# Kernel optimization log

Hardware: AMD Instinct MI355X
Metric: run time of the kernel (lower is better)

## Reference

```python
import jax, jax.numpy as jnp
import numpy as np

TEMPERATURE = 0.05


def setup_inputs() -> dict:
    key = jax.random.key(0)
    k1, k2, k3 = jax.random.split(key, 3)
    B, L, D = 4096, 32, 768
    image_features = jax.random.normal(k1, (B, D), dtype=jnp.float32)
    text_features = jax.random.normal(k2, (B, D), dtype=jnp.float32)
    labels = jax.random.randint(k3, (B, L), 0, 2, dtype=jnp.int64)
    return {"image_features": image_features, "text_features": text_features, "labels": labels}


def reference(image_features, text_features, labels):
    B, L = labels.shape
    num_logits = B
    # mask[i, j] = 1.0 iff labels[i, j] != 0; y[j] = outer(mask[:, j], mask[:, j])
    mask = (labels != 0).astype(jnp.float32)  # [B, L]
    # logit_scale = F.normalize(ones(L), p=2) * log(1/temp) -> every entry equal
    s = jnp.log(jnp.float32(1.0 / TEMPERATURE)) / jnp.sqrt(jnp.float32(L))
    logits_per_image = image_features @ text_features.T  # [B, B]
    logits_per_text = logits_per_image.T
    # All L scaled slices are identical (scale vector is constant), so one log_softmax each.
    pred_1 = jax.nn.log_softmax(s * logits_per_image, axis=-1)  # [B, B]
    pred_2 = jax.nn.log_softmax(s * logits_per_text, axis=-1)
    # kl_div(pred, y_j, 'sum') with 0/1 targets = -sum(y_j * pred)
    # sum_j m[:,j]^T P m[:,j] computed via two GEMMs without materializing [L,B,B]
    def masked_sum(pred):
        return jnp.einsum('jb,bj->', mask.T @ pred, mask)  # scalar
    loss_a = -masked_sum(pred_1) / num_logits
    loss_b = -masked_sum(pred_2) / num_logits
    total_loss = (loss_a + loss_b) / 2.0
    return total_loss / L
```

## Files before the change

kernel.cpp:

```cpp
#include <hip/hip_runtime.h>

#define NB 4096
#define DK 768
#define DKB 768
#define SCALE_S 0.5295756522f

typedef float f32x4 __attribute__((ext_vector_type(4)));
typedef int i32x4 __attribute__((ext_vector_type(4)));
typedef int i32x8 __attribute__((ext_vector_type(8)));

#define OFF_XQ      0u
#define OFF_YQ      3145728u
#define OFF_ROWPM   12582912u
#define OFF_ROWPS   13107200u
#define OFF_COLPM   13631488u
#define OFF_COLPS   14155776u
#define OFF_BITS    14712832u
#define OFF_CSPART  14729216u
#define OFF_DOTP    14731264u
#define OFF_WSUM    14735360u

static __device__ __forceinline__ unsigned char f2e4m3(float f) {
  union { float f; unsigned u; } x; x.f = f;
  unsigned s = (x.u >> 24) & 0x80u;
  x.u &= 0x7FFFFFFFu;
  float af = x.f;
  if (af >= 448.f) return (unsigned char)(s | 0x7Eu);
  int e = (int)(x.u >> 23) - 127;
  int eq = e < -6 ? -6 : e;
  float scale = __int_as_float((unsigned)((3 - eq) + 127) << 23);
  int q = (int)rintf(af * scale);
  if (q == 16) { q = 8; ++eq; }
  if (e < -6) return (unsigned char)(s | (unsigned)q);
  return (unsigned char)(s | (((unsigned)(eq + 7)) << 3) | ((unsigned)(q - 8)));
}

static __device__ __forceinline__ void gload16(const void* g, void* l) {
  __builtin_amdgcn_global_load_lds(
      (const __attribute__((address_space(1))) unsigned int*)g,
      (__attribute__((address_space(3))) unsigned int*)l,
      16, 0, 0);
}

__global__ void k_prep(const int* __restrict__ labels, unsigned* __restrict__ bits,
                       int* __restrict__ csPart,
                       const float* __restrict__ X, const float* __restrict__ Y,
                       unsigned char* __restrict__ Xq, unsigned char* __restrict__ Yq) {
  int t = threadIdx.x;
  if (blockIdx.x < 16) {
    __shared__ int cs[32];
    if (t < 32) cs[t] = 0;
    __syncthreads();
    int i = blockIdx.x * 256 + t;
    const int* row = labels + (size_t)i * 32;
    unsigned b = 0;
#pragma unroll
    for (int j = 0; j < 32; ++j) if (row[j] != 0) b |= (1u << j);
    bits[i] = b;
#pragma unroll
    for (int j = 0; j < 32; ++j) if (b & (1u << j)) atomicAdd(&cs[j], 1);
    __syncthreads();
    if (t < 32) csPart[blockIdx.x * 32 + t] = cs[t];
  } else {
    const int N4 = (NB * DK) / 4;
    const int stride = (gridDim.x - 16) * 256;
    for (int idx = (blockIdx.x - 16) * 256 + t; idx < 2 * N4; idx += stride) {
      float4 v; unsigned* dst;
      if (idx < N4) { v = ((const float4*)X)[idx]; dst = (unsigned*)Xq + idx; }
      else          { v = ((const float4*)Y)[idx - N4]; dst = (unsigned*)Yq + (idx - N4); }
      unsigned p = (unsigned)f2e4m3(v.x) | ((unsigned)f2e4m3(v.y) << 8) |
                   ((unsigned)f2e4m3(v.z) << 16) | ((unsigned)f2e4m3(v.w) << 24);
      *dst = p;
    }
  }
}


#define STAGE_T(DBUF, KT) do { \
    char* _lb = lds + (DBUF) * 65536 + lbOff; \
    const unsigned char* _g = pG + (size_t)(KT) * 128; \
    gload16(_g,                      _lb); \
    gload16(_g + (size_t)64  * DKB,  _lb + 8192); \
    gload16(_g + (size_t)128 * DKB,  _lb + 16384); \
    gload16(_g + (size_t)192 * DKB,  _lb + 24576); \
  } while (0)

#define LOADFRAG(DST, BASE) do { \
    i32x4 _lo = *(const i32x4*)((BASE) + offg0); \
    i32x4 _hi = *(const i32x4*)((BASE) + offg1); \
    DST[0] = _lo[0]; DST[1] = _lo[1]; DST[2] = _lo[2]; DST[3] = _lo[3]; \
    DST[4] = _hi[0]; DST[5] = _hi[1]; DST[6] = _hi[2]; DST[7] = _hi[3]; \
  } while (0)

__launch_bounds__(1024)
__global__ void k_gemm(const unsigned char* __restrict__ Xq,
                       const unsigned char* __restrict__ Yq,
                       const unsigned* __restrict__ bits,
                       float* __restrict__ rowPM, float* __restrict__ rowPS,
                       float* __restrict__ colPM, float* __restrict__ colPS,
                       float* __restrict__ dotPart) {
  extern __shared__ char lds[];

  const int t = threadIdx.x;
  const int wave = t >> 6, lane = t & 63;
  const int wr = wave >> 2, wc = wave & 3;

  const int bid = blockIdx.x;
  const int xcd = bid & 7, loc = bid >> 3;
  const int rb = (xcd & 3) * 4 + (loc >> 3);
  const int cb = (xcd >> 2) * 8 + (loc & 7);

  const int g0 = ((lane & 7) ^ (lane >> 3)) * 16;
  const int srow = (wave & 7) * 8 + (lane >> 3);
  const unsigned char* pG = (wave < 8)
      ? Xq + (size_t)(rb * 256 + srow) * DKB + g0
      : Yq + (size_t)(cb * 256 + srow) * DKB + g0;
  const int lbOff = ((wave < 8) ? 0 : 32768) + (wave & 7) * 1024;

  const int lrow = lane & 15;
  const int s7 = lrow & 7;
  const int gp = (lane >> 4) * 2;
  const int offg0 = ((gp) ^ s7) * 16;
  const int offg1 = ((gp + 1) ^ s7) * 16;
  const int rowA0 = (wr * 64 + lrow) * 128;
  const int rowB0 = 32768 + (wc * 64 + lrow) * 128;

  f32x4 acc[4][4];
#pragma unroll
  for (int m = 0; m < 4; ++m)
#pragma unroll
    for (int n = 0; n < 4; ++n) acc[m][n] = (f32x4){0.f, 0.f, 0.f, 0.f};

  STAGE_T(0, 0);
  asm volatile("s_waitcnt vmcnt(0)" ::: "memory");
  __builtin_amdgcn_s_barrier();

#pragma unroll 1
  for (int kt = 0; kt < 6; ++kt) {
    const int cur = kt & 1;
    if (kt < 5) STAGE_T(cur ^ 1, kt + 1);
    const char* _c = lds + cur * 65536;
    i32x8 bF[4];
#pragma unroll
    for (int n = 0; n < 4; ++n) LOADFRAG(bF[n], _c + rowB0 + n * 2048);
    __builtin_amdgcn_s_setprio(1);
#pragma unroll
    for (int m = 0; m < 4; ++m) {
      i32x8 aF;
      LOADFRAG(aF, _c + rowA0 + m * 2048);
#pragma unroll
      for (int n = 0; n < 4; ++n)
        acc[m][n] = __builtin_amdgcn_mfma_scale_f32_16x16x128_f8f6f4(
            aF, bF[n], acc[m][n], 0, 0, 0, 127, 0, 127);
    }
    __builtin_amdgcn_s_setprio(0);
    __syncthreads();
  }

  float* fb    = (float*)lds;
  float* redM  = fb;
  float* redS  = fb + 1024;
  float* redM2 = fb + 2048;
  float* redS2 = fb + 3072;
  unsigned* bR = (unsigned*)(fb + 4096);
  unsigned* bC = bR + 256;
  float* wred  = (float*)(bC + 256);

  if (t < 256) bR[t] = bits[rb * 256 + t];
  else if (t < 512) bC[t - 256] = bits[cb * 256 + (t - 256)];

#pragma unroll
  for (int m = 0; m < 4; ++m) {
#pragma unroll
    for (int r = 0; r < 4; ++r) {
      float v0 = SCALE_S * acc[m][0][r];
      float v1 = SCALE_S * acc[m][1][r];
      float v2 = SCALE_S * acc[m][2][r];
      float v3 = SCALE_S * acc[m][3][r];
      float mx = fmaxf(fmaxf(v0, v1), fmaxf(v2, v3));
#pragma unroll
      for (int off = 1; off < 16; off <<= 1) mx = fmaxf(mx, __shfl_xor(mx, off));
      float sm = __expf(v0 - mx) + __expf(v1 - mx) + __expf(v2 - mx) + __expf(v3 - mx);
#pragma unroll
      for (int off = 1; off < 16; off <<= 1) sm += __shfl_xor(sm, off);
      if ((lane & 15) == 0) {
        int row = wr * 64 + m * 16 + (lane >> 4) * 4 + r;
        redM[row * 4 + wc] = mx; redS[row * 4 + wc] = sm;
      }
    }
  }
#pragma unroll
  for (int n = 0; n < 4; ++n) {
    float mx = -3.0e38f;
#pragma unroll
    for (int m = 0; m < 4; ++m)
#pragma unroll
      for (int r = 0; r < 4; ++r) mx = fmaxf(mx, SCALE_S * acc[m][n][r]);
    mx = fmaxf(mx, __shfl_xor(mx, 16));
    mx = fmaxf(mx, __shfl_xor(mx, 32));
    float sm = 0.f;
#pragma unroll
    for (int m = 0; m < 4; ++m)
#pragma unroll
      for (int r = 0; r < 4; ++r) sm += __expf(SCALE_S * acc[m][n][r] - mx);
    sm += __shfl_xor(sm, 16);
    sm += __shfl_xor(sm, 32);
    if (lane < 16) {
      int col = wc * 64 + n * 16 + lane;
      redM2[col * 4 + wr] = mx; redS2[col * 4 + wr] = sm;
    }
  }
  __syncthreads();

  float ws = 0.f;
  {
    unsigned bc[4];
#pragma unroll
    for (int n = 0; n < 4; ++n) bc[n] = bC[wc * 64 + n * 16 + (lane & 15)];
#pragma unroll
    for (int m = 0; m < 4; ++m) {
#pragma unroll
      for (int r = 0; r < 4; ++r) {
        unsigned br = bR[wr * 64 + m * 16 + (lane >> 4) * 4 + r];
#pragma unroll
        for (int n = 0; n < 4; ++n)
          ws += (float)__popc(br & bc[n]) * acc[m][n][r];
      }
    }
  }
#pragma unroll
  for (int off = 32; off; off >>= 1) ws += __shfl_xor(ws, off);
  if (lane == 0) wred[wave] = ws;

  if (t < 256) {
    float M = fmaxf(fmaxf(redM[t * 4 + 0], redM[t * 4 + 1]),
                    fmaxf(redM[t * 4 + 2], redM[t * 4 + 3]));
    float S = 0.f;
#pragma unroll
    for (int k = 0; k < 4; ++k) S += redS[t * 4 + k] * __expf(redM[t * 4 + k] - M);
    rowPM[(size_t)cb * NB + rb * 256 + t] = M;
    rowPS[(size_t)cb * NB + rb * 256 + t] = S;
  } else if (t < 512) {
    int c = t - 256;
    float M = fmaxf(fmaxf(redM2[c * 4 + 0], redM2[c * 4 + 1]),
                    fmaxf(redM2[c * 4 + 2], redM2[c * 4 + 3]));
    float S = 0.f;
#pragma unroll
    for (int k = 0; k < 4; ++k) S += redS2[c * 4 + k] * __expf(redM2[c * 4 + k] - M);
    colPM[(size_t)rb * NB + cb * 256 + c] = M;
    colPS[(size_t)rb * NB + cb * 256 + c] = S;
  }
  __syncthreads();
  if (t == 0) {
    float s = 0.f;
#pragma unroll
    for (int w = 0; w < 16; ++w) s += wred[w];
    dotPart[bid] = s;
  }
}

__global__ void k_tail(const float* __restrict__ rowPM, const float* __restrict__ rowPS,
                       const float* __restrict__ colPM, const float* __restrict__ colPS,
                       const unsigned* __restrict__ bits, const int* __restrict__ csPart,
                       float* __restrict__ wsum) {
  __shared__ int cs[32];
  __shared__ float red[256];
  int t = threadIdx.x, b = blockIdx.x;
  if (t < 32) {
    int s = 0;
    for (int k = 0; k < 16; ++k) s += csPart[k * 32 + t];
    cs[t] = s;
  }
  __syncthreads();
  int g = b * 256 + t;
  int i; float M = -3.0e38f, S = 0.f;
  if (g < NB) {
    i = g;
#pragma unroll
    for (int c = 0; c < 16; ++c) M = fmaxf(M, rowPM[(size_t)c * NB + i]);
#pragma unroll
    for (int c = 0; c < 16; ++c) S += rowPS[(size_t)c * NB + i] * __expf(rowPM[(size_t)c * NB + i] - M);
  } else {
    i = g - NB;
#pragma unroll
    for (int c = 0; c < 16; ++c) M = fmaxf(M, colPM[(size_t)c * NB + i]);
#pragma unroll
    for (int c = 0; c < 16; ++c) S += colPS[(size_t)c * NB + i] * __expf(colPM[(size_t)c * NB + i] - M);
  }
  float lse = M + __logf(S);
  unsigned bb = bits[i];
  int rw = 0;
#pragma unroll
  for (int j = 0; j < 32; ++j) if (bb & (1u << j)) rw += cs[j];
  red[t] = (float)rw * lse;
  __syncthreads();
  for (int s = 128; s; s >>= 1) {
    if (t < s) red[t] += red[t + s];
    __syncthreads();
  }
  if (t == 0) wsum[b] = red[0];
}

__global__ void k_final(const float* __restrict__ wsum, const float* __restrict__ dotPart,
                        float* __restrict__ out) {
  __shared__ double red[256];
  int t = threadIdx.x;
  double a = 0.0;
  if (t < 32) a += (double)wsum[t];
  a -= 2.0 * (double)SCALE_S * (double)dotPart[t];
  red[t] = a;
  __syncthreads();
  for (int s = 128; s; s >>= 1) {
    if (t < s) red[t] += red[t + s];
    __syncthreads();
  }
  if (t == 0) out[0] = (float)(red[0] / (2.0 * (double)NB * 32.0));
}

extern "C" void kernel_launch(void* const* d_in, const int* in_sizes, int n_in,
                              void* d_out, int out_size, void* d_ws, size_t ws_size,
                              hipStream_t stream) {
  const float* X = (const float*)d_in[0];
  const float* Y = (const float*)d_in[1];
  const int* labels = (const int*)d_in[2];
  char* ws = (char*)d_ws;

  unsigned char* Xq = (unsigned char*)(ws + OFF_XQ);
  unsigned char* Yq = (unsigned char*)(ws + OFF_YQ);
  float* rowPM = (float*)(ws + OFF_ROWPM);
  float* rowPS = (float*)(ws + OFF_ROWPS);
  float* colPM = (float*)(ws + OFF_COLPM);
  float* colPS = (float*)(ws + OFF_COLPS);
  unsigned* bits = (unsigned*)(ws + OFF_BITS);
  int* csPart = (int*)(ws + OFF_CSPART);
  float* dotPart = (float*)(ws + OFF_DOTP);
  float* wsum = (float*)(ws + OFF_WSUM);

  (void)hipFuncSetAttribute((const void*)k_gemm,
                            hipFuncAttributeMaxDynamicSharedMemorySize, 131072);

  k_prep<<<1040, 256, 0, stream>>>(labels, bits, csPart, X, Y, Xq, Yq);
  k_gemm<<<256, 1024, 131072, stream>>>(Xq, Yq, bits, rowPM, rowPS, colPM, colPS, dotPart);
  k_tail<<<32, 256, 0, stream>>>(rowPM, rowPS, colPM, colPS, bits, csPart, wsum);
  k_final<<<1, 256, 0, stream>>>(wsum, dotPart, (float*)d_out);
}
```

Measured before the change: 41.68 us.

## Shrink GEMM tile to 256x128 with 512-thread blocks and single-buffered LDS

The fused FP8 GEMM/softmax-partials kernel goes from 256 blocks of 1024 threads on 256x256 tiles with double-buffered 128KB LDS to 512 blocks of 512 threads on 256x128 tiles with a single 48KB buffer. Launch bounds now target several resident blocks per CU, so latency is hidden by overlapping blocks instead of in-block prefetch. The reduction buffers, column-block indexing, tail loop count and final dotPart sum are resized to match the extra column blocks. In exchange, each block has two barriers per K step and no prefetch, and A tiles are loaded from global memory twice as often.

```diff
diff --git a/kernel.cpp b/kernel.cpp
--- a/kernel.cpp
+++ b/kernel.cpp
@@ -18,7 +18,7 @@
 #define OFF_BITS    14712832u
 #define OFF_CSPART  14729216u
 #define OFF_DOTP    14731264u
-#define OFF_WSUM    14735360u
+#define OFF_WSUM    14733312u
 
 static __device__ __forceinline__ unsigned char f2e4m3(float f) {
   union { float f; unsigned u; } x; x.f = f;
@@ -76,15 +76,6 @@
 }
 
 
-#define STAGE_T(DBUF, KT) do { \
-    char* _lb = lds + (DBUF) * 65536 + lbOff; \
-    const unsigned char* _g = pG + (size_t)(KT) * 128; \
-    gload16(_g,                      _lb); \
-    gload16(_g + (size_t)64  * DKB,  _lb + 8192); \
-    gload16(_g + (size_t)128 * DKB,  _lb + 16384); \
-    gload16(_g + (size_t)192 * DKB,  _lb + 24576); \
-  } while (0)
-
 #define LOADFRAG(DST, BASE) do { \
     i32x4 _lo = *(const i32x4*)((BASE) + offg0); \
     i32x4 _hi = *(const i32x4*)((BASE) + offg1); \
@@ -92,7 +83,18 @@
     DST[4] = _hi[0]; DST[5] = _hi[1]; DST[6] = _hi[2]; DST[7] = _hi[3]; \
   } while (0)
 
-__launch_bounds__(1024)
+#define STAGE_T(KT) do { \
+    const unsigned char* _ga = pA + (size_t)(KT) * 128; \
+    const unsigned char* _gb = pB + (size_t)(KT) * 128; \
+    gload16(_ga,                     ldsw); \
+    gload16(_ga + (size_t)64  * DKB, ldsw + 8192); \
+    gload16(_ga + (size_t)128 * DKB, ldsw + 16384); \
+    gload16(_ga + (size_t)192 * DKB, ldsw + 24576); \
+    gload16(_gb,                     ldsw + 32768); \
+    gload16(_gb + (size_t)64  * DKB, ldsw + 40960); \
+  } while (0)
+
+__launch_bounds__(512, 4)
 __global__ void k_gemm(const unsigned char* __restrict__ Xq,
                        const unsigned char* __restrict__ Yq,
                        const unsigned* __restrict__ bits,
@@ -103,19 +105,18 @@
 
   const int t = threadIdx.x;
   const int wave = t >> 6, lane = t & 63;
-  const int wr = wave >> 2, wc = wave & 3;
+  const int wr = wave >> 1, wc = wave & 1;
 
   const int bid = blockIdx.x;
   const int xcd = bid & 7, loc = bid >> 3;
-  const int rb = (xcd & 3) * 4 + (loc >> 3);
-  const int cb = (xcd >> 2) * 8 + (loc & 7);
+  const int rb = (xcd & 3) * 4 + (loc >> 4);
+  const int cb = (xcd >> 2) * 16 + (loc & 15);
 
   const int g0 = ((lane & 7) ^ (lane >> 3)) * 16;
-  const int srow = (wave & 7) * 8 + (lane >> 3);
-  const unsigned char* pG = (wave < 8)
-      ? Xq + (size_t)(rb * 256 + srow) * DKB + g0
-      : Yq + (size_t)(cb * 256 + srow) * DKB + g0;
-  const int lbOff = ((wave < 8) ? 0 : 32768) + (wave & 7) * 1024;
+  const int srow = wave * 8 + (lane >> 3);
+  const unsigned char* pA = Xq + (size_t)(rb * 256 + srow) * DKB + g0;
+  const unsigned char* pB = Yq + (size_t)(cb * 128 + srow) * DKB + g0;
+  char* ldsw = lds + wave * 1024;
 
   const int lrow = lane & 15;
   const int s7 = lrow & 7;
@@ -131,43 +132,39 @@
 #pragma unroll
     for (int n = 0; n < 4; ++n) acc[m][n] = (f32x4){0.f, 0.f, 0.f, 0.f};
 
-  STAGE_T(0, 0);
-  asm volatile("s_waitcnt vmcnt(0)" ::: "memory");
-  __builtin_amdgcn_s_barrier();
-
 #pragma unroll 1
   for (int kt = 0; kt < 6; ++kt) {
-    const int cur = kt & 1;
-    if (kt < 5) STAGE_T(cur ^ 1, kt + 1);
-    const char* _c = lds + cur * 65536;
+    __syncthreads();
+    STAGE_T(kt);
+    __syncthreads();
     i32x8 bF[4];
 #pragma unroll
-    for (int n = 0; n < 4; ++n) LOADFRAG(bF[n], _c + rowB0 + n * 2048);
+    for (int n = 0; n < 4; ++n) LOADFRAG(bF[n], lds + rowB0 + n * 2048);
     __builtin_amdgcn_s_setprio(1);
 #pragma unroll
     for (int m = 0; m < 4; ++m) {
       i32x8 aF;
-      LOADFRAG(aF, _c + rowA0 + m * 2048);
+      LOADFRAG(aF, lds + rowA0 + m * 2048);
 #pragma unroll
       for (int n = 0; n < 4; ++n)
         acc[m][n] = __builtin_amdgcn_mfma_scale_f32_16x16x128_f8f6f4(
             aF, bF[n], acc[m][n], 0, 0, 0, 127, 0, 127);
     }
     __builtin_amdgcn_s_setprio(0);
-    __syncthreads();
-  }
+  }
+  __syncthreads();
 
   float* fb    = (float*)lds;
   float* redM  = fb;
-  float* redS  = fb + 1024;
-  float* redM2 = fb + 2048;
-  float* redS2 = fb + 3072;
-  unsigned* bR = (unsigned*)(fb + 4096);
+  float* redS  = fb + 512;
+  float* redM2 = fb + 1024;
+  float* redS2 = fb + 1536;
+  unsigned* bR = (unsigned*)(fb + 2048);
   unsigned* bC = bR + 256;
-  float* wred  = (float*)(bC + 256);
+  float* wred  = (float*)(bC + 128);
 
   if (t < 256) bR[t] = bits[rb * 256 + t];
-  else if (t < 512) bC[t - 256] = bits[cb * 256 + (t - 256)];
+  else if (t < 384) bC[t - 256] = bits[cb * 128 + (t - 256)];
 
 #pragma unroll
   for (int m = 0; m < 4; ++m) {
@@ -185,7 +182,7 @@
       for (int off = 1; off < 16; off <<= 1) sm += __shfl_xor(sm, off);
       if ((lane & 15) == 0) {
         int row = wr * 64 + m * 16 + (lane >> 4) * 4 + r;
-        redM[row * 4 + wc] = mx; redS[row * 4 + wc] = sm;
+        redM[row * 2 + wc] = mx; redS[row * 2 + wc] = sm;
       }
     }
   }
@@ -233,28 +230,26 @@
   if (lane == 0) wred[wave] = ws;
 
   if (t < 256) {
-    float M = fmaxf(fmaxf(redM[t * 4 + 0], redM[t * 4 + 1]),
-                    fmaxf(redM[t * 4 + 2], redM[t * 4 + 3]));
-    float S = 0.f;
-#pragma unroll
-    for (int k = 0; k < 4; ++k) S += redS[t * 4 + k] * __expf(redM[t * 4 + k] - M);
+    float m0 = redM[t * 2 + 0], m1 = redM[t * 2 + 1];
+    float M = fmaxf(m0, m1);
+    float S = redS[t * 2 + 0] * __expf(m0 - M) + redS[t * 2 + 1] * __expf(m1 - M);
     rowPM[(size_t)cb * NB + rb * 256 + t] = M;
     rowPS[(size_t)cb * NB + rb * 256 + t] = S;
-  } else if (t < 512) {
+  } else if (t < 384) {
     int c = t - 256;
     float M = fmaxf(fmaxf(redM2[c * 4 + 0], redM2[c * 4 + 1]),
                     fmaxf(redM2[c * 4 + 2], redM2[c * 4 + 3]));
     float S = 0.f;
 #pragma unroll
     for (int k = 0; k < 4; ++k) S += redS2[c * 4 + k] * __expf(redM2[c * 4 + k] - M);
-    colPM[(size_t)rb * NB + cb * 256 + c] = M;
-    colPS[(size_t)rb * NB + cb * 256 + c] = S;
+    colPM[(size_t)rb * NB + cb * 128 + c] = M;
+    colPS[(size_t)rb * NB + cb * 128 + c] = S;
   }
   __syncthreads();
   if (t == 0) {
     float s = 0.f;
 #pragma unroll
-    for (int w = 0; w < 16; ++w) s += wred[w];
+    for (int w = 0; w < 8; ++w) s += wred[w];
     dotPart[bid] = s;
   }
 }
@@ -277,9 +272,9 @@
   if (g < NB) {
     i = g;
 #pragma unroll
-    for (int c = 0; c < 16; ++c) M = fmaxf(M, rowPM[(size_t)c * NB + i]);
-#pragma unroll
-    for (int c = 0; c < 16; ++c) S += rowPS[(size_t)c * NB + i] * __expf(rowPM[(size_t)c * NB + i] - M);
+    for (int c = 0; c < 32; ++c) M = fmaxf(M, rowPM[(size_t)c * NB + i]);
+#pragma unroll
+    for (int c = 0; c < 32; ++c) S += rowPS[(size_t)c * NB + i] * __expf(rowPM[(size_t)c * NB + i] - M);
   } else {
     i = g - NB;
 #pragma unroll
@@ -307,7 +302,7 @@
   int t = threadIdx.x;
   double a = 0.0;
   if (t < 32) a += (double)wsum[t];
-  a -= 2.0 * (double)SCALE_S * (double)dotPart[t];
+  a -= 2.0 * (double)SCALE_S * ((double)dotPart[t] + (double)dotPart[t + 256]);
   red[t] = a;
   __syncthreads();
   for (int s = 128; s; s >>= 1) {
@@ -337,10 +332,10 @@
   float* wsum = (float*)(ws + OFF_WSUM);
 
   (void)hipFuncSetAttribute((const void*)k_gemm,
-                            hipFuncAttributeMaxDynamicSharedMemorySize, 131072);
+                            hipFuncAttributeMaxDynamicSharedMemorySize, 49152);
 
   k_prep<<<1040, 256, 0, stream>>>(labels, bits, csPart, X, Y, Xq, Yq);
-  k_gemm<<<256, 1024, 131072, stream>>>(Xq, Yq, bits, rowPM, rowPS, colPM, colPS, dotPart);
+  k_gemm<<<512, 512, 49152, stream>>>(Xq, Yq, bits, rowPM, rowPS, colPM, colPS, dotPart);
   k_tail<<<32, 256, 0, stream>>>(rowPM, rowPS, colPM, colPS, bits, csPart, wsum);
   k_final<<<1, 256, 0, stream>>>(wsum, dotPart, (float*)d_out);
 }
```

New measurement: 43.58 us. +4.6%, slower.

## Quantize features to FP4 e2m1 and use FP4 scaled MFMA

Applied to the files above, without the earlier changes.

Replaces FP8 e4m3 quantization of the image and text features with unscaled FP4 e2m1 packing, eight values per word. The GEMM stages half as many bytes per K-tile into LDS, halves the shared memory footprint, and runs the scaled MFMA in FP4 mode. This cuts quantized-write and GEMM load traffic and MFMA cost. The risk is a large loss of accuracy, since unscaled FP4 represents normal-distributed inputs coarsely.

```diff
diff --git a/kernel.cpp b/kernel.cpp
--- a/kernel.cpp
+++ b/kernel.cpp
@@ -2,7 +2,7 @@
 
 #define NB 4096
 #define DK 768
-#define DKB 768
+#define DKB4 384
 #define SCALE_S 0.5295756522f
 
 typedef float f32x4 __attribute__((ext_vector_type(4)));
@@ -20,19 +20,19 @@
 #define OFF_DOTP    14731264u
 #define OFF_WSUM    14735360u
 
-static __device__ __forceinline__ unsigned char f2e4m3(float f) {
-  union { float f; unsigned u; } x; x.f = f;
-  unsigned s = (x.u >> 24) & 0x80u;
-  x.u &= 0x7FFFFFFFu;
-  float af = x.f;
-  if (af >= 448.f) return (unsigned char)(s | 0x7Eu);
-  int e = (int)(x.u >> 23) - 127;
-  int eq = e < -6 ? -6 : e;
-  float scale = __int_as_float((unsigned)((3 - eq) + 127) << 23);
-  int q = (int)rintf(af * scale);
-  if (q == 16) { q = 8; ++eq; }
-  if (e < -6) return (unsigned char)(s | (unsigned)q);
-  return (unsigned char)(s | (((unsigned)(eq + 7)) << 3) | ((unsigned)(q - 8)));
+static __device__ __forceinline__ unsigned f2e2m1(float f) {
+  unsigned s = f < 0.f ? 8u : 0u;
+  float a = fabsf(f);
+  unsigned c;
+  if      (a < 0.25f) c = 0;
+  else if (a < 0.75f) c = 1;
+  else if (a < 1.25f) c = 2;
+  else if (a < 1.75f) c = 3;
+  else if (a < 2.50f) c = 4;
+  else if (a < 3.50f) c = 5;
+  else if (a < 5.00f) c = 6;
+  else                c = 7;
+  return s | c;
 }
 
 static __device__ __forceinline__ void gload16(const void* g, void* l) {
@@ -45,7 +45,7 @@
 __global__ void k_prep(const int* __restrict__ labels, unsigned* __restrict__ bits,
                        int* __restrict__ csPart,
                        const float* __restrict__ X, const float* __restrict__ Y,
-                       unsigned char* __restrict__ Xq, unsigned char* __restrict__ Yq) {
+                       unsigned* __restrict__ Xq, unsigned* __restrict__ Yq) {
   int t = threadIdx.x;
   if (blockIdx.x < 16) {
     __shared__ int cs[32];
@@ -62,14 +62,17 @@
     __syncthreads();
     if (t < 32) csPart[blockIdx.x * 32 + t] = cs[t];
   } else {
-    const int N4 = (NB * DK) / 4;
+    const int N8 = (NB * DK) / 8;
     const int stride = (gridDim.x - 16) * 256;
-    for (int idx = (blockIdx.x - 16) * 256 + t; idx < 2 * N4; idx += stride) {
-      float4 v; unsigned* dst;
-      if (idx < N4) { v = ((const float4*)X)[idx]; dst = (unsigned*)Xq + idx; }
-      else          { v = ((const float4*)Y)[idx - N4]; dst = (unsigned*)Yq + (idx - N4); }
-      unsigned p = (unsigned)f2e4m3(v.x) | ((unsigned)f2e4m3(v.y) << 8) |
-                   ((unsigned)f2e4m3(v.z) << 16) | ((unsigned)f2e4m3(v.w) << 24);
+    for (int idx = (blockIdx.x - 16) * 256 + t; idx < 2 * N8; idx += stride) {
+      const float4* src; unsigned* dst; int base;
+      if (idx < N8) { base = idx;      src = (const float4*)X; dst = Xq + base; }
+      else          { base = idx - N8; src = (const float4*)Y; dst = Yq + base; }
+      float4 v0 = src[base * 2], v1 = src[base * 2 + 1];
+      unsigned p = f2e2m1(v0.x)        | (f2e2m1(v0.y) << 4)  |
+                   (f2e2m1(v0.z) << 8) | (f2e2m1(v0.w) << 12) |
+                   (f2e2m1(v1.x) << 16)| (f2e2m1(v1.y) << 20) |
+                   (f2e2m1(v1.z) << 24)| (f2e2m1(v1.w) << 28);
       *dst = p;
     }
   }
@@ -77,19 +80,9 @@
 
 
 #define STAGE_T(DBUF, KT) do { \
-    char* _lb = lds + (DBUF) * 65536 + lbOff; \
-    const unsigned char* _g = pG + (size_t)(KT) * 128; \
-    gload16(_g,                      _lb); \
-    gload16(_g + (size_t)64  * DKB,  _lb + 8192); \
-    gload16(_g + (size_t)128 * DKB,  _lb + 16384); \
-    gload16(_g + (size_t)192 * DKB,  _lb + 24576); \
-  } while (0)
-
-#define LOADFRAG(DST, BASE) do { \
-    i32x4 _lo = *(const i32x4*)((BASE) + offg0); \
-    i32x4 _hi = *(const i32x4*)((BASE) + offg1); \
-    DST[0] = _lo[0]; DST[1] = _lo[1]; DST[2] = _lo[2]; DST[3] = _lo[3]; \
-    DST[4] = _hi[0]; DST[5] = _hi[1]; DST[6] = _hi[2]; DST[7] = _hi[3]; \
+    char* _la = lds + (DBUF) * 32768 + wave * 1024; \
+    gload16(pA + (size_t)(KT) * 64, _la); \
+    gload16(pB + (size_t)(KT) * 64, _la + 16384); \
   } while (0)
 
 __launch_bounds__(1024)
@@ -110,20 +103,15 @@
   const int rb = (xcd & 3) * 4 + (loc >> 3);
   const int cb = (xcd >> 2) * 8 + (loc & 7);
 
-  const int g0 = ((lane & 7) ^ (lane >> 3)) * 16;
-  const int srow = (wave & 7) * 8 + (lane >> 3);
-  const unsigned char* pG = (wave < 8)
-      ? Xq + (size_t)(rb * 256 + srow) * DKB + g0
-      : Yq + (size_t)(cb * 256 + srow) * DKB + g0;
-  const int lbOff = ((wave < 8) ? 0 : 32768) + (wave & 7) * 1024;
+  const int gs = ((lane & 3) ^ ((lane >> 3) & 3)) * 16;
+  const int srow = wave * 16 + (lane >> 2);
+  const unsigned char* pA = Xq + (size_t)(rb * 256 + srow) * DKB4 + gs;
+  const unsigned char* pB = Yq + (size_t)(cb * 256 + srow) * DKB4 + gs;
 
   const int lrow = lane & 15;
-  const int s7 = lrow & 7;
-  const int gp = (lane >> 4) * 2;
-  const int offg0 = ((gp) ^ s7) * 16;
-  const int offg1 = ((gp + 1) ^ s7) * 16;
-  const int rowA0 = (wr * 64 + lrow) * 128;
-  const int rowB0 = 32768 + (wc * 64 + lrow) * 128;
+  const int offg = (((lane >> 4) ^ ((lrow >> 1) & 3))) * 16;
+  const int rowA0 = (wr * 64 + lrow) * 64 + offg;
+  const int rowB0 = 16384 + (wc * 64 + lrow) * 64 + offg;
 
   f32x4 acc[4][4];
 #pragma unroll
@@ -139,19 +127,25 @@
   for (int kt = 0; kt < 6; ++kt) {
     const int cur = kt & 1;
     if (kt < 5) STAGE_T(cur ^ 1, kt + 1);
-    const char* _c = lds + cur * 65536;
+    const char* _c = lds + cur * 32768;
     i32x8 bF[4];
 #pragma unroll
-    for (int n = 0; n < 4; ++n) LOADFRAG(bF[n], _c + rowB0 + n * 2048);
+    for (int n = 0; n < 4; ++n) {
+      i32x4 v = *(const i32x4*)(_c + rowB0 + n * 1024);
+      bF[n][0] = v[0]; bF[n][1] = v[1]; bF[n][2] = v[2]; bF[n][3] = v[3];
+      bF[n][4] = 0; bF[n][5] = 0; bF[n][6] = 0; bF[n][7] = 0;
+    }
     __builtin_amdgcn_s_setprio(1);
 #pragma unroll
     for (int m = 0; m < 4; ++m) {
+      i32x4 va = *(const i32x4*)(_c + rowA0 + m * 1024);
       i32x8 aF;
-      LOADFRAG(aF, _c + rowA0 + m * 2048);
+      aF[0] = va[0]; aF[1] = va[1]; aF[2] = va[2]; aF[3] = va[3];
+      aF[4] = 0; aF[5] = 0; aF[6] = 0; aF[7] = 0;
 #pragma unroll
       for (int n = 0; n < 4; ++n)
         acc[m][n] = __builtin_amdgcn_mfma_scale_f32_16x16x128_f8f6f4(
-            aF, bF[n], acc[m][n], 0, 0, 0, 127, 0, 127);
+            aF, bF[n], acc[m][n], 4, 4, 0, 127, 0, 127);
     }
     __builtin_amdgcn_s_setprio(0);
     __syncthreads();
@@ -325,8 +319,8 @@
   const int* labels = (const int*)d_in[2];
   char* ws = (char*)d_ws;
 
-  unsigned char* Xq = (unsigned char*)(ws + OFF_XQ);
-  unsigned char* Yq = (unsigned char*)(ws + OFF_YQ);
+  unsigned* Xq = (unsigned*)(ws + OFF_XQ);
+  unsigned* Yq = (unsigned*)(ws + OFF_YQ);
   float* rowPM = (float*)(ws + OFF_ROWPM);
   float* rowPS = (float*)(ws + OFF_ROWPS);
   float* colPM = (float*)(ws + OFF_COLPM);
@@ -337,10 +331,11 @@
   float* wsum = (float*)(ws + OFF_WSUM);
 
   (void)hipFuncSetAttribute((const void*)k_gemm,
-                            hipFuncAttributeMaxDynamicSharedMemorySize, 131072);
+                            hipFuncAttributeMaxDynamicSharedMemorySize, 65536);
 
   k_prep<<<1040, 256, 0, stream>>>(labels, bits, csPart, X, Y, Xq, Yq);
-  k_gemm<<<256, 1024, 131072, stream>>>(Xq, Yq, bits, rowPM, rowPS, colPM, colPS, dotPart);
+  k_gemm<<<256, 1024, 65536, stream>>>((const unsigned char*)Xq, (const unsigned char*)Yq,
+                                       bits, rowPM, rowPS, colPM, colPS, dotPart);
   k_tail<<<32, 256, 0, stream>>>(rowPM, rowPS, colPM, colPS, bits, csPart, wsum);
   k_final<<<1, 256, 0, stream>>>(wsum, dotPart, (float*)d_out);
 }
```

Result: faster. 36.98 us (median of 2 runs) (-11.3%).
